# Kernel optimization log

Measured on AMD Instinct MI355X. Metric: run time of the kernel, lower is better.

## Reference

```python
import jax, jax.numpy as jnp
import numpy as np

NEG_SLOPE = 0.2

def _lrelu(h):
    return jnp.where(h >= 0, h, NEG_SLOPE * h)

def _knn(x, k):
    # x: [B,N,C] -> idx [B,N,k] of smallest squared distances (self included)
    xx = jnp.sum(x * x, axis=-1)  # [B,N]
    d = xx[:, :, None] + xx[:, None, :] - 2.0 * jnp.einsum('bnc,bmc->bnm', x, x)
    return jax.lax.top_k(-d, k)[1]

def _edge_conv(x, k, w, s, t):
    # x: [B,N,C]; w: [O,2C]; s,t: [O] (eval BatchNorm folded to affine)
    idx = _knn(x, k)
    neigh = jax.vmap(lambda xb, ib: xb[ib])(x, idx)  # [B,N,k,C]
    xi = x[:, :, None, :]
    edge = jnp.concatenate([neigh - xi, jnp.broadcast_to(xi, neigh.shape)], axis=-1)  # [B,N,k,2C]
    h = _lrelu(jnp.einsum('bnkc,oc->bnko', edge, w) * s + t)
    return jnp.max(h, axis=2)  # [B,N,O]

def _pw(x, w, s, t):
    # pointwise conv1d(1x1) + folded BN + LeakyReLU; x: [B,N,Cin], w: [O,Cin]
    return _lrelu(jnp.einsum('bnc,oc->bno', x, w) * s + t)

def setup_inputs() -> dict:
    key = jax.random.key(0)
    ks = jax.random.split(key, 32)
    def w(i, o, c):
        return (jax.random.normal(ks[i], (o, c), jnp.float32) / np.sqrt(c)).astype(jnp.float32)
    def sc(i, o):
        return jax.random.uniform(ks[i], (o,), jnp.float32, 0.5, 1.5)
    def sh(i, o):
        return 0.05 * jax.random.normal(ks[i], (o,), jnp.float32)
    inp = {
        'xyz': jax.random.normal(ks[0], (8, 2048, 3), jnp.float32),
        'ec1_w': w(1, 64, 6),   'ec1_s': sc(2, 64),   'ec1_t': sh(3, 64),
        'ec2_w': w(4, 64, 128), 'ec2_s': sc(5, 64),   'ec2_t': sh(6, 64),
        'ec3_w': w(7, 128, 128),'ec3_s': sc(8, 128),  'ec3_t': sh(9, 128),
        'ec4_w': w(10, 256, 256),'ec4_s': sc(11, 256),'ec4_t': sh(12, 256),
        'fuse_w': w(13, 512, 512),'fuse_s': sc(14, 512),'fuse_t': sh(15, 512),
        'emb_w': w(16, 1024, 512),'emb_s': sc(17, 1024),'emb_t': sh(18, 1024),
        'h1_w': w(19, 256, 1536),'h1_s': sc(20, 256), 'h1_t': sh(21, 256),
        'h2_w': w(22, 256, 256), 'h2_s': sc(23, 256), 'h2_t': sh(24, 256),
        'h3_w': w(25, 13, 256),  'h3_b': sh(26, 13),
        'k': 20,
    }
    return inp

def reference(xyz, ec1_w, ec1_s, ec1_t, ec2_w, ec2_s, ec2_t, ec3_w, ec3_s, ec3_t,
              ec4_w, ec4_s, ec4_t, fuse_w, fuse_s, fuse_t, emb_w, emb_s, emb_t,
              h1_w, h1_s, h1_t, h2_w, h2_s, h2_t, h3_w, h3_b, k):
    B, N, _ = xyz.shape
    x1 = _edge_conv(xyz, k, ec1_w, ec1_s, ec1_t)   # [B,N,64]
    x2 = _edge_conv(x1, k, ec2_w, ec2_s, ec2_t)    # [B,N,64]
    x3 = _edge_conv(x2, k, ec3_w, ec3_s, ec3_t)    # [B,N,128]
    x4 = _edge_conv(x3, k, ec4_w, ec4_s, ec4_t)    # [B,N,256]
    x_cat = jnp.concatenate([x1, x2, x3, x4], axis=-1)  # [B,N,512]
    x_local = _pw(x_cat, fuse_w, fuse_s, fuse_t)        # [B,N,512]
    x_emb = _pw(x_local, emb_w, emb_s, emb_t)           # [B,N,1024]
    x_glob = jnp.max(x_emb, axis=1, keepdims=True)      # [B,1,1024]
    x_fin = jnp.concatenate([x_local, jnp.broadcast_to(x_glob, (B, N, x_glob.shape[-1]))], axis=-1)
    h = _pw(x_fin, h1_w, h1_s, h1_t)   # dropout is eval-mode identity
    h = _pw(h, h2_w, h2_s, h2_t)
    logits = jnp.einsum('bnc,oc->bno', h, h3_w) + h3_b  # [B,N,num_classes]
    return logits
```

## Files before the change

### kernel.cpp

```cpp
#include <hip/hip_runtime.h>
#include <utility>

#define B_  8
#define N_  2048
#define M_  16384
#define KNN 20
#define NEG 0.2f

__device__ __forceinline__ unsigned enc_f(float f) {
    unsigned u = __float_as_uint(f);
    return (u & 0x80000000u) ? ~u : (u | 0x80000000u);
}
__device__ __forceinline__ float dec_f(unsigned u) {
    return (u & 0x80000000u) ? __uint_as_float(u & 0x7FFFFFFFu) : __uint_as_float(~u);
}
__device__ __forceinline__ unsigned long long mkkey(unsigned e, unsigned j) {
    return ((unsigned long long)e << 32) | j;
}
__device__ __forceinline__ unsigned short bf_hi(float a) {
    unsigned u = __float_as_uint(a);
    unsigned r = u + 0x7FFFu + ((u >> 16) & 1u);
    return (unsigned short)(r >> 16);
}
__device__ __forceinline__ float bf_f(unsigned short h) {
    return __uint_as_float((unsigned)h << 16);
}

__global__ void wstack_kernel(const float* __restrict__ w, float* __restrict__ ws,
                              int O, int C, int Kp) {
    int i = blockIdx.x * 256 + threadIdx.x;
    if (i >= 2 * O * Kp) return;
    int row = i / Kp, k = i - row * Kp;
    float v = 0.f;
    if (k < C) {
        int o = (row < O) ? row : row - O;
        float w1 = w[(size_t)o * 2 * C + k];
        v = (row < O) ? w1 : (w[(size_t)o * 2 * C + C + k] - w1);
    }
    ws[i] = v;
}

__global__ void wsplit_kernel(const float* __restrict__ w, int ldin,
                              unsigned short* __restrict__ h, unsigned short* __restrict__ l,
                              int Kshift, int total) {
    int i = blockIdx.x * 256 + threadIdx.x;
    if (i >= total) return;
    int row = i >> Kshift, k = i & ((1 << Kshift) - 1);
    float v = w[(size_t)row * ldin + k];
    unsigned short hi = bf_hi(v);
    h[i] = hi;
    l[i] = bf_hi(v - bf_f(hi));
}

template<int C>
__global__ void prep_kernel(const float* __restrict__ x, int lda,
                            float* __restrict__ xx, float* __restrict__ xt) {
    int m = blockIdx.x * 256 + threadIdx.x;
    if (m >= M_) return;
    int b = m >> 11, n = m & 2047;
    const float* row = x + (size_t)m * lda;
    float s = 0.f;
#pragma unroll 8
    for (int c = 0; c < C; ++c) {
        float v = row[c];
        s = fmaf(v, v, s);
        xt[((size_t)b * C + c) * N_ + n] = v;
    }
    xx[m] = s;
}

#define RM 8
template<int C>
__global__ __launch_bounds__(512, 4) void dist_topk_kernel(
        const float* __restrict__ xt, const float* __restrict__ xx,
        int* __restrict__ idxout) {
    constexpr int C4 = (C + 3) & ~3;
    __shared__ float xi[RM][C4];
    __shared__ unsigned m4s[RM][512];
    __shared__ unsigned long long cand[RM][128];
    __shared__ int cnt[RM];
    __shared__ unsigned tub[RM];
    int blk = blockIdx.x;
    int b = blk >> 8;
    int i0 = (blk & 255) * RM;
    int tid = threadIdx.x;
    int lane = tid & 63, r = tid >> 6;
    const float* xtb = xt + (size_t)b * C * N_;
    const float* xxb = xx + (size_t)b * N_;

    for (int t = tid; t < RM * C4; t += 512) {
        int rr = t / C4, c = t - rr * C4;
        xi[rr][c] = (c < C) ? xtb[(size_t)c * N_ + (i0 + rr)] : 0.f;
    }
    if (tid < RM) cnt[tid] = 0;
    __syncthreads();

    float xxir[RM];
#pragma unroll
    for (int q = 0; q < RM; ++q) xxir[q] = xxb[i0 + q];
    float xxj[4];
#pragma unroll
    for (int p = 0; p < 4; ++p) xxj[p] = xxb[tid + 512 * p];

    float acc[RM][4];
#pragma unroll
    for (int q = 0; q < RM; ++q)
#pragma unroll
        for (int p = 0; p < 4; ++p) acc[q][p] = 0.f;

#pragma unroll 4
    for (int c = 0; c < C; ++c) {
        float xtv[4];
#pragma unroll
        for (int p = 0; p < 4; ++p) xtv[p] = xtb[(size_t)c * N_ + tid + 512 * p];
#pragma unroll
        for (int q = 0; q < RM; ++q) {
            float a = xi[q][c];
#pragma unroll
            for (int p = 0; p < 4; ++p) acc[q][p] = fmaf(a, xtv[p], acc[q][p]);
        }
    }

#pragma unroll
    for (int q = 0; q < RM; ++q) {
        unsigned m = 0xFFFFFFFFu;
#pragma unroll
        for (int p = 0; p < 4; ++p) {
            unsigned e = enc_f(xxir[q] + xxj[p] - 2.f * acc[q][p]);
            m = (e < m) ? e : m;
        }
        m4s[q][tid] = m;
    }
    __syncthreads();

    {
        unsigned lmin = 0xFFFFFFFFu;
#pragma unroll
        for (int i = 0; i < 8; ++i) {
            unsigned v = m4s[r][lane + 64 * i];
            lmin = (v < lmin) ? v : lmin;
        }
        unsigned T = 0u;
        for (int bpos = 31; bpos >= 0; --bpos) {
            unsigned cd = T | (1u << bpos);
            unsigned long long bal = __ballot(lmin < cd);
            if ((int)__popcll(bal) < KNN) T = cd;
        }
        if (lane == 0) tub[r] = T;
    }
    __syncthreads();

#pragma unroll
    for (int q = 0; q < RM; ++q) {
        unsigned Tq = tub[q];
#pragma unroll
        for (int p = 0; p < 4; ++p) {
            unsigned e = enc_f(xxir[q] + xxj[p] - 2.f * acc[q][p]);
            if (e <= Tq) {
                int pos = atomicAdd(&cnt[q], 1);
                if (pos < 128)
                    cand[q][pos] = mkkey(e, (unsigned)(tid + 512 * p));
            }
        }
    }
    __syncthreads();

    int A = cnt[r];
    if (A > 128) A = 128;
    int* orow = idxout + (size_t)(b * N_ + i0 + r) * KNN;
    for (int cc = lane; cc < A; cc += 64) {
        unsigned long long mykey = cand[r][cc];
        int rank = 0;
        for (int i = 0; i < A; ++i)
            rank += (cand[r][i] < mykey) ? 1 : 0;
        if (rank < KNN) orow[rank] = (int)(mykey & 2047u);
    }
}

typedef __attribute__((ext_vector_type(8))) short short8;
typedef __attribute__((ext_vector_type(4))) float f32x4;

template<int MODE>
__global__ __launch_bounds__(256, 2) void mgemm_kernel(
        const float* __restrict__ A, int lda,
        const unsigned short* __restrict__ Bh, const unsigned short* __restrict__ Bl, int ldw,
        float* __restrict__ out, int ldo,
        const float* __restrict__ sc, const float* __restrict__ sh,
        const float* __restrict__ addvec, unsigned* __restrict__ gmax,
        int K, int O) {
    __shared__ unsigned short Ah_s[128][40];
    __shared__ unsigned short Al_s[128][40];
    __shared__ unsigned short Bh_s[128][40];
    __shared__ unsigned short Bl_s[128][40];
    int tid = threadIdx.x;
    int lane = tid & 63, w = tid >> 6;
    int ln = lane & 15, kg = lane >> 4;
    int wm = (w >> 1) * 64, wn = (w & 1) * 64;
    int m0 = blockIdx.y * 128, o0 = blockIdx.x * 128;
    f32x4 acc[4][4] = {};

    for (int k0 = 0; k0 < K; k0 += 32) {
#pragma unroll
        for (int j = 0; j < 4; ++j) {
            int s = tid + j * 256;
            int row = s >> 3, q = s & 7;
            float4 v = *(const float4*)&A[(size_t)(m0 + row) * lda + k0 + q * 4];
            unsigned short h0 = bf_hi(v.x), h1 = bf_hi(v.y), h2 = bf_hi(v.z), h3 = bf_hi(v.w);
            unsigned short l0 = bf_hi(v.x - bf_f(h0)), l1 = bf_hi(v.y - bf_f(h1));
            unsigned short l2 = bf_hi(v.z - bf_f(h2)), l3 = bf_hi(v.w - bf_f(h3));
            *(uint2*)&Ah_s[row][q * 4] = make_uint2((unsigned)h0 | ((unsigned)h1 << 16),
                                                    (unsigned)h2 | ((unsigned)h3 << 16));
            *(uint2*)&Al_s[row][q * 4] = make_uint2((unsigned)l0 | ((unsigned)l1 << 16),
                                                    (unsigned)l2 | ((unsigned)l3 << 16));
        }
#pragma unroll
        for (int j = 0; j < 2; ++j) {
            int s = tid + j * 256;
            int row = s >> 2, q = s & 3;
            *(uint4*)&Bh_s[row][q * 8] = *(const uint4*)&Bh[(size_t)(o0 + row) * ldw + k0 + q * 8];
            *(uint4*)&Bl_s[row][q * 8] = *(const uint4*)&Bl[(size_t)(o0 + row) * ldw + k0 + q * 8];
        }
        __syncthreads();

        short8 ah[4], al[4], bh[4], bl[4];
#pragma unroll
        for (int t = 0; t < 4; ++t) {
            ah[t] = *(const short8*)&Ah_s[wm + t * 16 + ln][kg * 8];
            al[t] = *(const short8*)&Al_s[wm + t * 16 + ln][kg * 8];
            bh[t] = *(const short8*)&Bh_s[wn + t * 16 + ln][kg * 8];
            bl[t] = *(const short8*)&Bl_s[wn + t * 16 + ln][kg * 8];
        }
#pragma unroll
        for (int t = 0; t < 4; ++t)
#pragma unroll
            for (int u = 0; u < 4; ++u) {
                acc[t][u] = __builtin_amdgcn_mfma_f32_16x16x32_bf16(ah[t], bh[u], acc[t][u], 0, 0, 0);
                acc[t][u] = __builtin_amdgcn_mfma_f32_16x16x32_bf16(ah[t], bl[u], acc[t][u], 0, 0, 0);
                acc[t][u] = __builtin_amdgcn_mfma_f32_16x16x32_bf16(al[t], bh[u], acc[t][u], 0, 0, 0);
            }
        __syncthreads();
    }

    int b = m0 >> 11;
    if constexpr (MODE == 3) {
#pragma unroll
        for (int u = 0; u < 4; ++u) {
            int o = o0 + wn + u * 16 + ln;
            float s = sc[o], t0 = sh[o];
            float cm = -1e30f;
#pragma unroll
            for (int t = 0; t < 4; ++t)
#pragma unroll
                for (int p = 0; p < 4; ++p) {
                    float v = fmaf(acc[t][u][p], s, t0);
                    v = (v >= 0.f) ? v : NEG * v;
                    cm = fmaxf(cm, v);
                }
            cm = fmaxf(cm, __shfl_xor(cm, 16));
            cm = fmaxf(cm, __shfl_xor(cm, 32));
            if (kg == 0) atomicMax(&gmax[b * 1024 + o], enc_f(cm));
        }
        return;
    }
#pragma unroll
    for (int t = 0; t < 4; ++t)
#pragma unroll
        for (int p = 0; p < 4; ++p) {
            int m = m0 + wm + t * 16 + kg * 4 + p;
#pragma unroll
            for (int u = 0; u < 4; ++u) {
                int o = o0 + wn + u * 16 + ln;
                float v = acc[t][u][p];
                if (MODE == 1) {
                    if (addvec) v += addvec[b * O + o];
                    v = fmaf(v, sc[o], sh[o]);
                    v = (v >= 0.f) ? v : NEG * v;
                }
                out[(size_t)m * ldo + o] = v;
            }
        }
}

template<int TN, int MODE, bool VEC>
__global__ __launch_bounds__(256, 4) void gemm_kernel(
        const float* __restrict__ A, int lda,
        const float* __restrict__ W, int ldw,
        float* __restrict__ out, int ldo,
        const float* __restrict__ sc, const float* __restrict__ sh,
        const float* __restrict__ addvec, unsigned* __restrict__ gmax,
        int K, int O) {
    constexpr int TM = 128;
    constexpr int JN = TN / 16;
    __shared__ float As[16][TM];
    __shared__ float Bs[16][TN];
    int tid = threadIdx.x;
    int tx = tid & 15, ty = tid >> 4;
    int o0 = blockIdx.x * TN, m0 = blockIdx.y * TM;
    float acc[8][JN] = {};

    for (int k0 = 0; k0 < K; k0 += 16) {
        if constexpr (VEC) {
#pragma unroll
            for (int s = 0; s < 2; ++s) {
                int t = tid + s * 256;
                int row = t >> 2, c4 = (t & 3) << 2;
                float4 v = *(const float4*)&A[(size_t)(m0 + row) * lda + k0 + c4];
                As[c4 + 0][row] = v.x; As[c4 + 1][row] = v.y;
                As[c4 + 2][row] = v.z; As[c4 + 3][row] = v.w;
            }
#pragma unroll
            for (int s = 0; s < TN / 64; ++s) {
                int t = tid + s * 256;
                int row = t >> 2, c4 = (t & 3) << 2;
                int o = o0 + row;
                float4 v = make_float4(0.f, 0.f, 0.f, 0.f);
                if (o < O) v = *(const float4*)&W[(size_t)o * ldw + k0 + c4];
                Bs[c4 + 0][row] = v.x; Bs[c4 + 1][row] = v.y;
                Bs[c4 + 2][row] = v.z; Bs[c4 + 3][row] = v.w;
            }
        } else {
            for (int t = tid; t < TM * 16; t += 256) {
                int row = t >> 4, k = t & 15;
                As[k][row] = (k0 + k < K) ? A[(size_t)(m0 + row) * lda + k0 + k] : 0.f;
            }
            for (int t = tid; t < TN * 16; t += 256) {
                int row = t >> 4, k = t & 15;
                Bs[k][row] = W[(size_t)(o0 + row) * ldw + k0 + k];
            }
        }
        __syncthreads();
#pragma unroll
        for (int kk = 0; kk < 16; ++kk) {
            float a[8], bv[JN];
            *(float4*)&a[0] = *(const float4*)&As[kk][ty * 8];
            *(float4*)&a[4] = *(const float4*)&As[kk][ty * 8 + 4];
            *(float4*)&bv[0] = *(const float4*)&Bs[kk][tx * JN];
            if (JN == 8) *(float4*)&bv[4] = *(const float4*)&Bs[kk][tx * JN + 4];
#pragma unroll
            for (int i = 0; i < 8; ++i)
#pragma unroll
                for (int j = 0; j < JN; ++j)
                    acc[i][j] = fmaf(a[i], bv[j], acc[i][j]);
        }
        __syncthreads();
    }

    int b = m0 >> 11;
    bool fullstore = (o0 + TN <= O) && ((ldo & 3) == 0);
#pragma unroll
    for (int i = 0; i < 8; ++i) {
        int m = m0 + ty * 8 + i;
        float vals[JN];
#pragma unroll
        for (int j = 0; j < JN; ++j) {
            int o = o0 + tx * JN + j;
            float v = acc[i][j];
            if (MODE == 1) {
                if (addvec) v += addvec[b * O + o];
                v = fmaf(v, sc[o], sh[o]);
                v = (v >= 0.f) ? v : NEG * v;
            } else if (MODE == 2) {
                v += sh[o];
            }
            vals[j] = v;
        }
        if (fullstore) {
#pragma unroll
            for (int j0 = 0; j0 < JN; j0 += 4)
                *(float4*)&out[(size_t)m * ldo + o0 + tx * JN + j0] = *(float4*)&vals[j0];
        } else {
#pragma unroll
            for (int j = 0; j < JN; ++j) {
                int o = o0 + tx * JN + j;
                if (o < O) out[(size_t)m * ldo + o] = vals[j];
            }
        }
    }
}

__global__ void edge_max_kernel(const float* __restrict__ yz, const int* __restrict__ idx,
                                const float* __restrict__ sc, const float* __restrict__ sh,
                                float* __restrict__ out, int ldo, int oshift) {
    int gid = blockIdx.x * 256 + threadIdx.x;
    int O = 1 << oshift;
    int m = gid >> (oshift - 2);
    int o = (gid & ((1 << (oshift - 2)) - 1)) << 2;
    int ldyz = 2 * O;
    float4 z = *(const float4*)&yz[(size_t)m * ldyz + O + o];
    float4 s4 = *(const float4*)&sc[o];
    float4 t4 = *(const float4*)&sh[o];
    const int* ip = idx + (size_t)m * KNN;
    int bbase = m & ~(N_ - 1);
    float4 mv = make_float4(-1e30f, -1e30f, -1e30f, -1e30f);
#pragma unroll
    for (int kk = 0; kk < KNN; ++kk) {
        int j = ip[kk];
        float4 y = *(const float4*)&yz[(size_t)(bbase + j) * ldyz + o];
        float v;
        v = fmaf(y.x + z.x, s4.x, t4.x); v = (v >= 0.f) ? v : NEG * v; mv.x = fmaxf(mv.x, v);
        v = fmaf(y.y + z.y, s4.y, t4.y); v = (v >= 0.f) ? v : NEG * v; mv.y = fmaxf(mv.y, v);
        v = fmaf(y.z + z.z, s4.z, t4.z); v = (v >= 0.f) ? v : NEG * v; mv.z = fmaxf(mv.z, v);
        v = fmaf(y.w + z.w, s4.w, t4.w); v = (v >= 0.f) ? v : NEG * v; mv.w = fmaxf(mv.w, v);
    }
    *(float4*)&out[(size_t)m * ldo + o] = mv;
}

__global__ void init_gmax_kernel(unsigned* __restrict__ g) {
    int i = blockIdx.x * 256 + threadIdx.x;
    if (i < B_ * 1024) g[i] = enc_f(-1e30f);
}
__global__ void decode_gmax_kernel(const unsigned* __restrict__ g, float* __restrict__ glob) {
    int i = blockIdx.x * 256 + threadIdx.x;
    if (i < B_ * 1024) glob[i] = dec_f(g[i]);
}

__global__ void corr_kernel(const float* __restrict__ glob, const float* __restrict__ h1w,
                            float* __restrict__ corr) {
    int wid = (blockIdx.x * 256 + threadIdx.x) >> 6;
    int lane = threadIdx.x & 63;
    int b = wid >> 8, o = wid & 255;
    const float* g = glob + b * 1024;
    const float* w = h1w + (size_t)o * 1536 + 512;
    float s = 0.f;
    for (int c = lane; c < 1024; c += 64) s = fmaf(g[c], w[c], s);
#pragma unroll
    for (int off = 32; off >= 1; off >>= 1) s += __shfl_xor(s, off);
    if (lane == 0) corr[b * 256 + o] = s;
}

extern "C" void kernel_launch(void* const* d_in, const int* in_sizes, int n_in,
                              void* d_out, int out_size, void* d_ws, size_t ws_size,
                              hipStream_t stream) {
    const float* xyz    = (const float*)d_in[0];
    const float* ec1_w  = (const float*)d_in[1];
    const float* ec1_s  = (const float*)d_in[2];
    const float* ec1_t  = (const float*)d_in[3];
    const float* ec2_w  = (const float*)d_in[4];
    const float* ec2_s  = (const float*)d_in[5];
    const float* ec2_t  = (const float*)d_in[6];
    const float* ec3_w  = (const float*)d_in[7];
    const float* ec3_s  = (const float*)d_in[8];
    const float* ec3_t  = (const float*)d_in[9];
    const float* ec4_w  = (const float*)d_in[10];
    const float* ec4_s  = (const float*)d_in[11];
    const float* ec4_t  = (const float*)d_in[12];
    const float* fuse_w = (const float*)d_in[13];
    const float* fuse_s = (const float*)d_in[14];
    const float* fuse_t = (const float*)d_in[15];
    const float* emb_w  = (const float*)d_in[16];
    const float* emb_s  = (const float*)d_in[17];
    const float* emb_t  = (const float*)d_in[18];
    const float* h1_w   = (const float*)d_in[19];
    const float* h1_s   = (const float*)d_in[20];
    const float* h1_t   = (const float*)d_in[21];
    const float* h2_w   = (const float*)d_in[22];
    const float* h2_s   = (const float*)d_in[23];
    const float* h2_t   = (const float*)d_in[24];
    const float* h3_w   = (const float*)d_in[25];
    const float* h3_b   = (const float*)d_in[26];
    float* out = (float*)d_out;

    float* ws = (float*)d_ws;
    size_t off = 0;
    float* xcat = ws + off; off += (size_t)M_ * 512;
    float* xloc = ws + off; off += (size_t)M_ * 512;
    float* yz   = ws + off; off += (size_t)M_ * 512;
    float* xt   = ws + off; off += (size_t)B_ * 128 * N_;
    float* xx   = ws + off; off += M_;
    int*   idx  = (int*)(ws + off); off += (size_t)M_ * KNN;
    float* ws1  = ws + off; off += 2 * 64 * 16;
    float* ws2  = ws + off; off += 2 * 64 * 64;
    float* ws3  = ws + off; off += 2 * 128 * 64;
    float* ws4  = ws + off; off += 2 * 256 * 128;
    unsigned* gmax = (unsigned*)(ws + off); off += B_ * 1024;
    float* glob = ws + off; off += B_ * 1024;
    float* corr = ws + off; off += B_ * 256;
    unsigned short* fuse_h = (unsigned short*)(ws + off); off += 512 * 512 / 2;
    unsigned short* fuse_l = (unsigned short*)(ws + off); off += 512 * 512 / 2;
    unsigned short* emb_h  = (unsigned short*)(ws + off); off += 1024 * 512 / 2;
    unsigned short* emb_l  = (unsigned short*)(ws + off); off += 1024 * 512 / 2;
    unsigned short* h1_h   = (unsigned short*)(ws + off); off += 256 * 512 / 2;
    unsigned short* h1_l   = (unsigned short*)(ws + off); off += 256 * 512 / 2;
    unsigned short* h2_h   = (unsigned short*)(ws + off); off += 256 * 256 / 2;
    unsigned short* h2_l   = (unsigned short*)(ws + off); off += 256 * 256 / 2;
    unsigned short* ws4_h  = (unsigned short*)(ws + off); off += 512 * 128 / 2;
    unsigned short* ws4_l  = (unsigned short*)(ws + off); off += 512 * 128 / 2;
    float* h1o  = yz;
    float* h2o  = yz + (size_t)M_ * 256;

    wstack_kernel<<<(2 * 64 * 16 + 255) / 256, 256, 0, stream>>>(ec1_w, ws1, 64, 3, 16);
    wstack_kernel<<<(2 * 64 * 64 + 255) / 256, 256, 0, stream>>>(ec2_w, ws2, 64, 64, 64);
    wstack_kernel<<<(2 * 128 * 64 + 255) / 256, 256, 0, stream>>>(ec3_w, ws3, 128, 64, 64);
    wstack_kernel<<<(2 * 256 * 128 + 255) / 256, 256, 0, stream>>>(ec4_w, ws4, 256, 128, 128);
    wsplit_kernel<<<(512 * 512 + 255) / 256, 256, 0, stream>>>(fuse_w, 512, fuse_h, fuse_l, 9, 512 * 512);
    wsplit_kernel<<<(1024 * 512 + 255) / 256, 256, 0, stream>>>(emb_w, 512, emb_h, emb_l, 9, 1024 * 512);
    wsplit_kernel<<<(256 * 512 + 255) / 256, 256, 0, stream>>>(h1_w, 1536, h1_h, h1_l, 9, 256 * 512);
    wsplit_kernel<<<(256 * 256 + 255) / 256, 256, 0, stream>>>(h2_w, 256, h2_h, h2_l, 8, 256 * 256);
    wsplit_kernel<<<(512 * 128 + 255) / 256, 256, 0, stream>>>(ws4, 128, ws4_h, ws4_l, 7, 512 * 128);

    prep_kernel<3><<<M_ / 256, 256, 0, stream>>>(xyz, 3, xx, xt);
    dist_topk_kernel<3><<<M_ / RM, 512, 0, stream>>>(xt, xx, idx);
    gemm_kernel<128, 0, false><<<dim3(1, M_ / 128), 256, 0, stream>>>(xyz, 3, ws1, 16, yz, 128, nullptr, nullptr, nullptr, nullptr, 3, 128);
    edge_max_kernel<<<(M_ * 16) / 256, 256, 0, stream>>>(yz, idx, ec1_s, ec1_t, xcat + 0, 512, 6);

    prep_kernel<64><<<M_ / 256, 256, 0, stream>>>(xcat + 0, 512, xx, xt);
    dist_topk_kernel<64><<<M_ / RM, 512, 0, stream>>>(xt, xx, idx);
    gemm_kernel<64, 0, true><<<dim3(2, M_ / 128), 256, 0, stream>>>(xcat + 0, 512, ws2, 64, yz, 128, nullptr, nullptr, nullptr, nullptr, 64, 128);
    edge_max_kernel<<<(M_ * 16) / 256, 256, 0, stream>>>(yz, idx, ec2_s, ec2_t, xcat + 64, 512, 6);

    prep_kernel<64><<<M_ / 256, 256, 0, stream>>>(xcat + 64, 512, xx, xt);
    dist_topk_kernel<64><<<M_ / RM, 512, 0, stream>>>(xt, xx, idx);
    gemm_kernel<128, 0, true><<<dim3(2, M_ / 128), 256, 0, stream>>>(xcat + 64, 512, ws3, 64, yz, 256, nullptr, nullptr, nullptr, nullptr, 64, 256);
    edge_max_kernel<<<(M_ * 32) / 256, 256, 0, stream>>>(yz, idx, ec3_s, ec3_t, xcat + 128, 512, 7);

    prep_kernel<128><<<M_ / 256, 256, 0, stream>>>(xcat + 128, 512, xx, xt);
    dist_topk_kernel<128><<<M_ / RM, 512, 0, stream>>>(xt, xx, idx);
    mgemm_kernel<0><<<dim3(4, M_ / 128), 256, 0, stream>>>(xcat + 128, 512, ws4_h, ws4_l, 128, yz, 512, nullptr, nullptr, nullptr, nullptr, 128, 512);
    edge_max_kernel<<<(M_ * 64) / 256, 256, 0, stream>>>(yz, idx, ec4_s, ec4_t, xcat + 256, 512, 8);

    mgemm_kernel<1><<<dim3(4, M_ / 128), 256, 0, stream>>>(xcat, 512, fuse_h, fuse_l, 512, xloc, 512, fuse_s, fuse_t, nullptr, nullptr, 512, 512);

    init_gmax_kernel<<<32, 256, 0, stream>>>(gmax);
    mgemm_kernel<3><<<dim3(8, M_ / 128), 256, 0, stream>>>(xloc, 512, emb_h, emb_l, 512, nullptr, 0, emb_s, emb_t, nullptr, gmax, 512, 1024);
    decode_gmax_kernel<<<32, 256, 0, stream>>>(gmax, glob);
    corr_kernel<<<512, 256, 0, stream>>>(glob, h1_w, corr);

    mgemm_kernel<1><<<dim3(2, M_ / 128), 256, 0, stream>>>(xloc, 512, h1_h, h1_l, 512, h1o, 256, h1_s, h1_t, corr, nullptr, 512, 256);
    mgemm_kernel<1><<<dim3(2, M_ / 128), 256, 0, stream>>>(h1o, 256, h2_h, h2_l, 256, h2o, 256, h2_s, h2_t, nullptr, nullptr, 256, 256);
    gemm_kernel<64, 2, true><<<dim3(1, M_ / 128), 256, 0, stream>>>(h2o, 256, h3_w, 256, out, 13, nullptr, h3_b, nullptr, nullptr, 256, 13);
}
```

Before: 788.8 us.

## Retile kNN distance kernel to 8 columns per thread and merge weight-prep launches

The distance/top-k kernel now uses 256 threads per block, each handling 8 contiguous columns with float4 loads and a 4-channel register-blocked inner loop that reads xi rows as float4. This raises the FMA count per load and gives vectorised global access, at the cost of more registers and each wave handling two rows in the selection phase. Separately, the nine weight stacking and splitting kernels plus the gmax init are fused into one launch, and gmax decoding is folded into corr_kernel, which removes several small launches.

```diff
diff --git a/kernel.cpp b/kernel.cpp
--- a/kernel.cpp
+++ b/kernel.cpp
@@ -1,5 +1,4 @@
 #include <hip/hip_runtime.h>
-#include <utility>
 
 #define B_  8
 #define N_  2048
@@ -26,30 +25,62 @@
     return __uint_as_float((unsigned)h << 16);
 }
 
-__global__ void wstack_kernel(const float* __restrict__ w, float* __restrict__ ws,
-                              int O, int C, int Kp) {
-    int i = blockIdx.x * 256 + threadIdx.x;
+__device__ __forceinline__ void wstack_body(const float* __restrict__ w, float* __restrict__ ws,
+                                            int O, int Cc, int Kp, int i) {
     if (i >= 2 * O * Kp) return;
     int row = i / Kp, k = i - row * Kp;
     float v = 0.f;
-    if (k < C) {
+    if (k < Cc) {
         int o = (row < O) ? row : row - O;
-        float w1 = w[(size_t)o * 2 * C + k];
-        v = (row < O) ? w1 : (w[(size_t)o * 2 * C + C + k] - w1);
+        float w1 = w[(size_t)o * 2 * Cc + k];
+        v = (row < O) ? w1 : (w[(size_t)o * 2 * Cc + Cc + k] - w1);
     }
     ws[i] = v;
 }
-
-__global__ void wsplit_kernel(const float* __restrict__ w, int ldin,
-                              unsigned short* __restrict__ h, unsigned short* __restrict__ l,
-                              int Kshift, int total) {
-    int i = blockIdx.x * 256 + threadIdx.x;
-    if (i >= total) return;
+__device__ __forceinline__ void wsplit_body(const float* __restrict__ w, int ldin,
+                                            unsigned short* __restrict__ h, unsigned short* __restrict__ l,
+                                            int Kshift, int i) {
     int row = i >> Kshift, k = i & ((1 << Kshift) - 1);
     float v = w[(size_t)row * ldin + k];
     unsigned short hi = bf_hi(v);
     h[i] = hi;
     l[i] = bf_hi(v - bf_f(hi));
+}
+__device__ __forceinline__ void wstacksplit_body(const float* __restrict__ w,
+                                                 unsigned short* __restrict__ h, unsigned short* __restrict__ l,
+                                                 int i) {
+    int row = i >> 7, k = i & 127;
+    int o = (row < 256) ? row : row - 256;
+    float w1 = w[(size_t)o * 256 + k];
+    float v = (row < 256) ? w1 : (w[(size_t)o * 256 + 128 + k] - w1);
+    unsigned short hi = bf_hi(v);
+    h[i] = hi;
+    l[i] = bf_hi(v - bf_f(hi));
+}
+
+__global__ void prep_weights_kernel(
+        const float* __restrict__ ec1_w, const float* __restrict__ ec2_w,
+        const float* __restrict__ ec3_w, const float* __restrict__ ec4_w,
+        const float* __restrict__ fuse_w, const float* __restrict__ emb_w,
+        const float* __restrict__ h1_w, const float* __restrict__ h2_w,
+        float* __restrict__ ws1, float* __restrict__ ws2, float* __restrict__ ws3,
+        unsigned short* __restrict__ ws4_h, unsigned short* __restrict__ ws4_l,
+        unsigned short* __restrict__ fuse_h, unsigned short* __restrict__ fuse_l,
+        unsigned short* __restrict__ emb_h, unsigned short* __restrict__ emb_l,
+        unsigned short* __restrict__ h1_h, unsigned short* __restrict__ h1_l,
+        unsigned short* __restrict__ h2_h, unsigned short* __restrict__ h2_l,
+        unsigned* __restrict__ gmax) {
+    int blk = blockIdx.x, tid = threadIdx.x;
+    if (blk < 8)            { wstack_body(ec1_w, ws1, 64, 3, 16, blk * 256 + tid); }
+    else if (blk < 40)      { wstack_body(ec2_w, ws2, 64, 64, 64, (blk - 8) * 256 + tid); }
+    else if (blk < 104)     { wstack_body(ec3_w, ws3, 128, 64, 64, (blk - 40) * 256 + tid); }
+    else if (blk < 360)     { wstacksplit_body(ec4_w, ws4_h, ws4_l, (blk - 104) * 256 + tid); }
+    else if (blk < 1384)    { wsplit_body(fuse_w, 512, fuse_h, fuse_l, 9, (blk - 360) * 256 + tid); }
+    else if (blk < 3432)    { wsplit_body(emb_w, 512, emb_h, emb_l, 9, (blk - 1384) * 256 + tid); }
+    else if (blk < 3944)    { wsplit_body(h1_w, 1536, h1_h, h1_l, 9, (blk - 3432) * 256 + tid); }
+    else if (blk < 4200)    { wsplit_body(h2_w, 256, h2_h, h2_l, 8, (blk - 3944) * 256 + tid); }
+    else                    { int i = (blk - 4200) * 256 + tid;
+                              if (i < B_ * 1024) gmax[i] = enc_f(-1e30f); }
 }
 
 template<int C>
@@ -71,12 +102,12 @@
 
 #define RM 8
 template<int C>
-__global__ __launch_bounds__(512, 4) void dist_topk_kernel(
+__global__ __launch_bounds__(256, 3) void dist_topk_kernel(
         const float* __restrict__ xt, const float* __restrict__ xx,
         int* __restrict__ idxout) {
     constexpr int C4 = (C + 3) & ~3;
     __shared__ float xi[RM][C4];
-    __shared__ unsigned m4s[RM][512];
+    __shared__ unsigned m4s[RM][256];
     __shared__ unsigned long long cand[RM][128];
     __shared__ int cnt[RM];
     __shared__ unsigned tub[RM];
@@ -84,11 +115,11 @@
     int b = blk >> 8;
     int i0 = (blk & 255) * RM;
     int tid = threadIdx.x;
-    int lane = tid & 63, r = tid >> 6;
+    int lane = tid & 63, w = tid >> 6;
     const float* xtb = xt + (size_t)b * C * N_;
     const float* xxb = xx + (size_t)b * N_;
 
-    for (int t = tid; t < RM * C4; t += 512) {
+    for (int t = tid; t < RM * C4; t += 256) {
         int rr = t / C4, c = t - rr * C4;
         xi[rr][c] = (c < C) ? xtb[(size_t)c * N_ + (i0 + rr)] : 0.f;
     }
@@ -98,26 +129,39 @@
     float xxir[RM];
 #pragma unroll
     for (int q = 0; q < RM; ++q) xxir[q] = xxb[i0 + q];
-    float xxj[4];
-#pragma unroll
-    for (int p = 0; p < 4; ++p) xxj[p] = xxb[tid + 512 * p];
-
-    float acc[RM][4];
+    float xxj[8];
+    *(float4*)&xxj[0] = *(const float4*)&xxb[8 * tid];
+    *(float4*)&xxj[4] = *(const float4*)&xxb[8 * tid + 4];
+
+    float acc[RM][8];
 #pragma unroll
     for (int q = 0; q < RM; ++q)
 #pragma unroll
-        for (int p = 0; p < 4; ++p) acc[q][p] = 0.f;
-
-#pragma unroll 4
-    for (int c = 0; c < C; ++c) {
-        float xtv[4];
-#pragma unroll
-        for (int p = 0; p < 4; ++p) xtv[p] = xtb[(size_t)c * N_ + tid + 512 * p];
+        for (int p = 0; p < 8; ++p) acc[q][p] = 0.f;
+
+    int j0 = 8 * tid;
+    for (int c0 = 0; c0 < C4; c0 += 4) {
+        float xa[4][8];
+#pragma unroll
+        for (int e = 0; e < 4; ++e) {
+            int c = c0 + e;
+            if (c < C) {
+                *(float4*)&xa[e][0] = *(const float4*)&xtb[(size_t)c * N_ + j0];
+                *(float4*)&xa[e][4] = *(const float4*)&xtb[(size_t)c * N_ + j0 + 4];
+            } else {
+#pragma unroll
+                for (int p = 0; p < 8; ++p) xa[e][p] = 0.f;
+            }
+        }
 #pragma unroll
         for (int q = 0; q < RM; ++q) {
-            float a = xi[q][c];
-#pragma unroll
-            for (int p = 0; p < 4; ++p) acc[q][p] = fmaf(a, xtv[p], acc[q][p]);
+            float4 xiq = *(const float4*)&xi[q][c0];
+            float av[4] = {xiq.x, xiq.y, xiq.z, xiq.w};
+#pragma unroll
+            for (int e = 0; e < 4; ++e)
+#pragma unroll
+                for (int p = 0; p < 8; ++p)
+                    acc[q][p] = fmaf(av[e], xa[e][p], acc[q][p]);
         }
     }
 
@@ -125,7 +169,7 @@
     for (int q = 0; q < RM; ++q) {
         unsigned m = 0xFFFFFFFFu;
 #pragma unroll
-        for (int p = 0; p < 4; ++p) {
+        for (int p = 0; p < 8; ++p) {
             unsigned e = enc_f(xxir[q] + xxj[p] - 2.f * acc[q][p]);
             m = (e < m) ? e : m;
         }
@@ -133,11 +177,12 @@
     }
     __syncthreads();
 
-    {
+    for (int rr = 0; rr < 2; ++rr) {
+        int q = 2 * w + rr;
         unsigned lmin = 0xFFFFFFFFu;
 #pragma unroll
-        for (int i = 0; i < 8; ++i) {
-            unsigned v = m4s[r][lane + 64 * i];
+        for (int i = 0; i < 4; ++i) {
+            unsigned v = m4s[q][lane + 64 * i];
             lmin = (v < lmin) ? v : lmin;
         }
         unsigned T = 0u;
@@ -146,7 +191,7 @@
             unsigned long long bal = __ballot(lmin < cd);
             if ((int)__popcll(bal) < KNN) T = cd;
         }
-        if (lane == 0) tub[r] = T;
+        if (lane == 0) tub[q] = T;
     }
     __syncthreads();
 
@@ -154,26 +199,29 @@
     for (int q = 0; q < RM; ++q) {
         unsigned Tq = tub[q];
 #pragma unroll
-        for (int p = 0; p < 4; ++p) {
+        for (int p = 0; p < 8; ++p) {
             unsigned e = enc_f(xxir[q] + xxj[p] - 2.f * acc[q][p]);
             if (e <= Tq) {
                 int pos = atomicAdd(&cnt[q], 1);
                 if (pos < 128)
-                    cand[q][pos] = mkkey(e, (unsigned)(tid + 512 * p));
+                    cand[q][pos] = mkkey(e, (unsigned)(j0 + p));
             }
         }
     }
     __syncthreads();
 
-    int A = cnt[r];
-    if (A > 128) A = 128;
-    int* orow = idxout + (size_t)(b * N_ + i0 + r) * KNN;
-    for (int cc = lane; cc < A; cc += 64) {
-        unsigned long long mykey = cand[r][cc];
-        int rank = 0;
-        for (int i = 0; i < A; ++i)
-            rank += (cand[r][i] < mykey) ? 1 : 0;
-        if (rank < KNN) orow[rank] = (int)(mykey & 2047u);
+    for (int rr = 0; rr < 2; ++rr) {
+        int q = 2 * w + rr;
+        int A = cnt[q];
+        if (A > 128) A = 128;
+        int* orow = idxout + (size_t)(b * N_ + i0 + q) * KNN;
+        for (int cc = lane; cc < A; cc += 64) {
+            unsigned long long mykey = cand[q][cc];
+            int rank = 0;
+            for (int i = 0; i < A; ++i)
+                rank += (cand[q][i] < mykey) ? 1 : 0;
+            if (rank < KNN) orow[rank] = (int)(mykey & 2047u);
+        }
     }
 }
 
@@ -405,24 +453,15 @@
     *(float4*)&out[(size_t)m * ldo + o] = mv;
 }
 
-__global__ void init_gmax_kernel(unsigned* __restrict__ g) {
-    int i = blockIdx.x * 256 + threadIdx.x;
-    if (i < B_ * 1024) g[i] = enc_f(-1e30f);
-}
-__global__ void decode_gmax_kernel(const unsigned* __restrict__ g, float* __restrict__ glob) {
-    int i = blockIdx.x * 256 + threadIdx.x;
-    if (i < B_ * 1024) glob[i] = dec_f(g[i]);
-}
-
-__global__ void corr_kernel(const float* __restrict__ glob, const float* __restrict__ h1w,
+__global__ void corr_kernel(const unsigned* __restrict__ gmax, const float* __restrict__ h1w,
                             float* __restrict__ corr) {
     int wid = (blockIdx.x * 256 + threadIdx.x) >> 6;
     int lane = threadIdx.x & 63;
     int b = wid >> 8, o = wid & 255;
-    const float* g = glob + b * 1024;
+    const unsigned* g = gmax + b * 1024;
     const float* w = h1w + (size_t)o * 1536 + 512;
     float s = 0.f;
-    for (int c = lane; c < 1024; c += 64) s = fmaf(g[c], w[c], s);
+    for (int c = lane; c < 1024; c += 64) s = fmaf(dec_f(g[c]), w[c], s);
 #pragma unroll
     for (int off = 32; off >= 1; off >>= 1) s += __shfl_xor(s, off);
     if (lane == 0) corr[b * 256 + o] = s;
@@ -471,9 +510,7 @@
     float* ws1  = ws + off; off += 2 * 64 * 16;
     float* ws2  = ws + off; off += 2 * 64 * 64;
     float* ws3  = ws + off; off += 2 * 128 * 64;
-    float* ws4  = ws + off; off += 2 * 256 * 128;
     unsigned* gmax = (unsigned*)(ws + off); off += B_ * 1024;
-    float* glob = ws + off; off += B_ * 1024;
     float* corr = ws + off; off += B_ * 256;
     unsigned short* fuse_h = (unsigned short*)(ws + off); off += 512 * 512 / 2;
     unsigned short* fuse_l = (unsigned short*)(ws + off); off += 512 * 512 / 2;
@@ -488,42 +525,35 @@
     float* h1o  = yz;
     float* h2o  = yz + (size_t)M_ * 256;
 
-    wstack_kernel<<<(2 * 64 * 16 + 255) / 256, 256, 0, stream>>>(ec1_w, ws1, 64, 3, 16);
-    wstack_kernel<<<(2 * 64 * 64 + 255) / 256, 256, 0, stream>>>(ec2_w, ws2, 64, 64, 64);
-    wstack_kernel<<<(2 * 128 * 64 + 255) / 256, 256, 0, stream>>>(ec3_w, ws3, 128, 64, 64);
-    wstack_kernel<<<(2 * 256 * 128 + 255) / 256, 256, 0, stream>>>(ec4_w, ws4, 256, 128, 128);
-    wsplit_kernel<<<(512 * 512 + 255) / 256, 256, 0, stream>>>(fuse_w, 512, fuse_h, fuse_l, 9, 512 * 512);
-    wsplit_kernel<<<(1024 * 512 + 255) / 256, 256, 0, stream>>>(emb_w, 512, emb_h, emb_l, 9, 1024 * 512);
-    wsplit_kernel<<<(256 * 512 + 255) / 256, 256, 0, stream>>>(h1_w, 1536, h1_h, h1_l, 9, 256 * 512);
-    wsplit_kernel<<<(256 * 256 + 255) / 256, 256, 0, stream>>>(h2_w, 256, h2_h, h2_l, 8, 256 * 256);
-    wsplit_kernel<<<(512 * 128 + 255) / 256, 256, 0, stream>>>(ws4, 128, ws4_h, ws4_l, 7, 512 * 128);
+    prep_weights_kernel<<<4232, 256, 0, stream>>>(
+        ec1_w, ec2_w, ec3_w, ec4_w, fuse_w, emb_w, h1_w, h2_w,
+        ws1, ws2, ws3, ws4_h, ws4_l, fuse_h, fuse_l, emb_h, emb_l,
+        h1_h, h1_l, h2_h, h2_l, gmax);
 
     prep_kernel<3><<<M_ / 256, 256, 0, stream>>>(xyz, 3, xx, xt);
-    dist_topk_kernel<3><<<M_ / RM, 512, 0, stream>>>(xt, xx, idx);
+    dist_topk_kernel<3><<<M_ / RM, 256, 0, stream>>>(xt, xx, idx);
     gemm_kernel<128, 0, false><<<dim3(1, M_ / 128), 256, 0, stream>>>(xyz, 3, ws1, 16, yz, 128, nullptr, nullptr, nullptr, nullptr, 3, 128);
     edge_max_kernel<<<(M_ * 16) / 256, 256, 0, stream>>>(yz, idx, ec1_s, ec1_t, xcat + 0, 512, 6);
 
     prep_kernel<64><<<M_ / 256, 256, 0, stream>>>(xcat + 0, 512, xx, xt);
-    dist_topk_kernel<64><<<M_ / RM, 512, 0, stream>>>(xt, xx, idx);
+    dist_topk_kernel<64><<<M_ / RM, 256, 0, stream>>>(xt, xx, idx);
     gemm_kernel<64, 0, true><<<dim3(2, M_ / 128), 256, 0, stream>>>(xcat + 0, 512, ws2, 64, yz, 128, nullptr, nullptr, nullptr, nullptr, 64, 128);
     edge_max_kernel<<<(M_ * 16) / 256, 256, 0, stream>>>(yz, idx, ec2_s, ec2_t, xcat + 64, 512, 6);
 
     prep_kernel<64><<<M_ / 256, 256, 0, stream>>>(xcat + 64, 512, xx, xt);
-    dist_topk_kernel<64><<<M_ / RM, 512, 0, stream>>>(xt, xx, idx);
+    dist_topk_kernel<64><<<M_ / RM, 256, 0, stream>>>(xt, xx, idx);
     gemm_kernel<128, 0, true><<<dim3(2, M_ / 128), 256, 0, stream>>>(xcat + 64, 512, ws3, 64, yz, 256, nullptr, nullptr, nullptr, nullptr, 64, 256);
     edge_max_kernel<<<(M_ * 32) / 256, 256, 0, stream>>>(yz, idx, ec3_s, ec3_t, xcat + 128, 512, 7);
 
     prep_kernel<128><<<M_ / 256, 256, 0, stream>>>(xcat + 128, 512, xx, xt);
-    dist_topk_kernel<128><<<M_ / RM, 512, 0, stream>>>(xt, xx, idx);
+    dist_topk_kernel<128><<<M_ / RM, 256, 0, stream>>>(xt, xx, idx);
     mgemm_kernel<0><<<dim3(4, M_ / 128), 256, 0, stream>>>(xcat + 128, 512, ws4_h, ws4_l, 128, yz, 512, nullptr, nullptr, nullptr, nullptr, 128, 512);
     edge_max_kernel<<<(M_ * 64) / 256, 256, 0, stream>>>(yz, idx, ec4_s, ec4_t, xcat + 256, 512, 8);
 
     mgemm_kernel<1><<<dim3(4, M_ / 128), 256, 0, stream>>>(xcat, 512, fuse_h, fuse_l, 512, xloc, 512, fuse_s, fuse_t, nullptr, nullptr, 512, 512);
 
-    init_gmax_kernel<<<32, 256, 0, stream>>>(gmax);
     mgemm_kernel<3><<<dim3(8, M_ / 128), 256, 0, stream>>>(xloc, 512, emb_h, emb_l, 512, nullptr, 0, emb_s, emb_t, nullptr, gmax, 512, 1024);
-    decode_gmax_kernel<<<32, 256, 0, stream>>>(gmax, glob);
-    corr_kernel<<<512, 256, 0, stream>>>(glob, h1_w, corr);
+    corr_kernel<<<512, 256, 0, stream>>>(gmax, h1_w, corr);
 
     mgemm_kernel<1><<<dim3(2, M_ / 128), 256, 0, stream>>>(xloc, 512, h1_h, h1_l, 512, h1o, 256, h1_s, h1_t, corr, nullptr, 512, 256);
     mgemm_kernel<1><<<dim3(2, M_ / 128), 256, 0, stream>>>(h1o, 256, h2_h, h2_l, 256, h2o, 256, h2_s, h2_t, nullptr, nullptr, 256, 256);
```

Measured after the change: 861.3 us. 9.2% more time.
